# Optimization experiments

Measured on AMD Instinct MI355X. Metric: run time of the kernel, lower is better.

## Reference

```python
import jax, jax.numpy as jnp
import numpy as np

# dims (see shape_source)
N = 100000          # num_ent
E = 400000          # num edges
B = 2048            # batch of (sub, rel) queries
INIT_DIM = 100
UFD = 100           # user_fe_dim
ENT_DIM = INIT_DIM + 3 * UFD   # feature_method='concat' -> 400
H = 2               # attention heads
D = 64              # per-head dim
GCN = H * D         # gcn_dim = embed_dim = 128 (gcn_layer == 1)
NUM_REL = 50
NR2 = 2 * NUM_REL


def setup_inputs() -> dict:
    key = jax.random.key(0)
    ks = jax.random.split(key, 17)
    inp = {}
    # constructor / forward int tensors
    inp["edge_index"] = jax.random.randint(ks[0], (2, E), 0, N, dtype=jnp.int32)
    inp["edge_type"] = jax.random.randint(ks[1], (E,), 0, NR2, dtype=jnp.int32)
    inp["edge_type_p"] = jax.random.randint(ks[2], (E,), 0, NR2, dtype=jnp.int32)
    inp["ent_feature"] = jax.random.randint(ks[3], (N, 3), 0, 3, dtype=jnp.int32)
    inp["sub"] = jax.random.randint(ks[4], (B,), 0, N, dtype=jnp.int32)
    inp["rel"] = jax.random.randint(ks[5], (B,), 0, NR2, dtype=jnp.int32)
    inp["relp"] = jax.random.randint(ks[6], (B,), 0, NR2, dtype=jnp.int32)
    # learned parameters
    s = 0.02
    inp["id_embed"] = jax.random.normal(ks[7], (N, INIT_DIM), jnp.float32) * s
    inp["gender_tab"] = jax.random.normal(ks[8], (3, UFD), jnp.float32) * s
    inp["age_tab"] = jax.random.normal(ks[9], (9, UFD), jnp.float32) * s
    inp["level_tab"] = jax.random.normal(ks[10], (11, UFD), jnp.float32) * s
    inp["init_rel"] = jax.random.normal(ks[11], (NR2, ENT_DIM), jnp.float32) * s
    inp["W"] = jax.random.normal(ks[12], (ENT_DIM, H * D), jnp.float32) * 0.05
    inp["Wr"] = jax.random.normal(ks[13], (ENT_DIM, H * D), jnp.float32) * 0.05
    inp["att_src"] = jax.random.normal(ks[14], (H, D), jnp.float32) * 0.05
    inp["att_dst"] = jax.random.normal(ks[15], (H, D), jnp.float32) * 0.05
    inp["Wrel"] = jax.random.normal(ks[16], (ENT_DIM, GCN), jnp.float32) * 0.05
    return inp


def _segment_softmax(logits, seg, num_segments):
    # logits: [E, H], seg: [E] destination node ids
    m = jax.ops.segment_max(logits, seg, num_segments=num_segments)
    ex = jnp.exp(logits - m[seg])
    den = jax.ops.segment_sum(ex, seg, num_segments=num_segments)
    return ex / (den[seg] + 1e-16)


def _rghat_conv(x, rel_emb, edge_index, edge_type, W, Wr, att_src, att_dst, Wrel):
    # relational multi-head graph attention (RGHATConv)
    n = x.shape[0]
    h = (x @ W).reshape(n, H, D)                       # [N,H,D] projected nodes
    r_proj = (rel_emb @ Wr).reshape(-1, H, D)          # [R,H,D]
    src, dst = edge_index[0], edge_index[1]
    msg = h[src] + r_proj[edge_type]                   # [E,H,D] edge messages
    logits = jax.nn.leaky_relu(
        jnp.sum(msg * att_src, axis=-1) + jnp.sum(h[dst] * att_dst, axis=-1),
        negative_slope=0.2,
    )                                                  # [E,H]
    alpha = _segment_softmax(logits, dst, n)           # per-destination softmax
    out = jax.ops.segment_sum(alpha[..., None] * msg, dst, num_segments=n)
    out = jnp.tanh(out.reshape(n, H * D))              # [N,GCN]
    r_out = rel_emb @ Wrel                             # [R,GCN]
    return out, r_out


def reference(edge_index, edge_type, edge_type_p, ent_feature, sub, rel, relp,
              id_embed, gender_tab, age_tab, level_tab, init_rel,
              W, Wr, att_src, att_dst, Wrel):
    # feature_method == 'concat': gather per-node feature embeddings and concat
    x1 = gender_tab[ent_feature[:, 0]]
    x2 = age_tab[ent_feature[:, 1]]
    x3 = level_tab[ent_feature[:, 2]]
    init_embed = jnp.concatenate([id_embed, x1, x2, x3], axis=1)  # [N, ENT_DIM]
    # single conv layer (gcn_layer == 1); dropouts are identity in eval
    x, r = _rghat_conv(init_embed, init_rel, edge_index, edge_type,
                       W, Wr, att_src, att_dst, Wrel)
    sub_emb = x[sub]                                   # index_select gather
    # add_parent_rel == False -> r returned whole (relp unused)
    return (sub_emb, r, x)
```

## Files before the change

kernel.cpp:

```cpp
#include <hip/hip_runtime.h>
#include <hip/hip_bf16.h>
#include <hip/hip_fp16.h>

#define N_NODES 100000
#define E_EDGES 400000
#define B_SUB 2048
#define INIT_DIM 100
#define UFD 100
#define ENT_DIM 400
#define GCN 128
#define NR2 100
#define KPAD 416
#define NCH 13
#define CAP 64

typedef __attribute__((ext_vector_type(8))) short shortx8;
typedef __attribute__((ext_vector_type(4))) float floatx4;

#define OUT_R_OFF ((long)B_SUB * GCN)
#define OUT_X_OFF ((long)(B_SUB + NR2) * GCN)

__device__ __forceinline__ unsigned short f2b(float f) {
    unsigned u = __float_as_uint(f);
    u += 0x7fffu + ((u >> 16) & 1u);
    return (unsigned short)(u >> 16);
}
__device__ __forceinline__ unsigned pk2(float x, float y) {
    return (unsigned)f2b(x) | ((unsigned)f2b(y) << 16);
}
__device__ __forceinline__ float blo(unsigned u) { return __uint_as_float(u << 16); }
__device__ __forceinline__ float bhi(unsigned u) { return __uint_as_float(u & 0xFFFF0000u); }

__global__ void wt_kernel(const float* __restrict__ W, unsigned short* __restrict__ Wt,
                          int* __restrict__ cursor) {
    int idx = blockIdx.x * 256 + threadIdx.x;
    if (idx < GCN * KPAD) {
        int n = idx & 127, k = idx >> 7;
        unsigned short o = 0;
        if (k < ENT_DIM) o = f2b(W[(long)k * GCN + n]);
        Wt[(long)n * KPAD + k] = o;
    }
    if (idx < N_NODES) cursor[idx] = 0;
}

__global__ void rel_kernel(const float* __restrict__ init_rel, const float* __restrict__ Wr,
                           const float* __restrict__ Wrel, const float* __restrict__ att_src,
                           unsigned* __restrict__ rp_b, float* __restrict__ rproj_att,
                           float* __restrict__ out_r) {
    int rel = blockIdx.x;
    int tx = threadIdx.x;
    __shared__ float rl[ENT_DIM];
    __shared__ float accbuf[128];
    for (int k = tx; k < ENT_DIM; k += 128) rl[k] = init_rel[(long)rel * ENT_DIM + k];
    __syncthreads();
    float acc1 = 0.f, acc2 = 0.f;
    for (int k = 0; k < ENT_DIM; ++k) {
        float v = rl[k];
        acc1 += v * Wr[(long)k * GCN + tx];
        acc2 += v * Wrel[(long)k * GCN + tx];
    }
    out_r[rel * GCN + tx] = acc2;
    accbuf[tx] = acc1;
    int head = tx >> 6, d = tx & 63;
    float v = acc1 * att_src[head * 64 + d];
    for (int off = 32; off > 0; off >>= 1) v += __shfl_down(v, off, 64);
    if (d == 0) rproj_att[rel * 2 + head] = v;
    __syncthreads();
    if (tx < 64) rp_b[rel * 64 + tx] = pk2(accbuf[tx], accbuf[tx + 64]);
}

__device__ __forceinline__ float4 load_seg(const float* __restrict__ id_embed,
                                           const float* __restrict__ gtab,
                                           const float* __restrict__ atab,
                                           const float* __restrict__ ltab,
                                           int n, int f0, int f1, int f2, int kg) {
    if (kg < 100)      return *(const float4*)&id_embed[(long)n * INIT_DIM + kg];
    else if (kg < 200) return *(const float4*)&gtab[f0 * UFD + kg - 100];
    else if (kg < 300) return *(const float4*)&atab[f1 * UFD + kg - 200];
    else if (kg < 400) return *(const float4*)&ltab[f2 * UFD + kg - 300];
    return make_float4(0.f, 0.f, 0.f, 0.f);
}

__global__ __launch_bounds__(256) void hgemm_kernel(
        const float* __restrict__ id_embed, const float* __restrict__ gtab,
        const float* __restrict__ atab, const float* __restrict__ ltab,
        const int* __restrict__ ent_feature, const unsigned short* __restrict__ Wt,
        const float* __restrict__ att_src, const float* __restrict__ att_dst,
        unsigned* __restrict__ h_b, float* __restrict__ hsrc_att, float* __restrict__ hdst_att) {
    __shared__ __align__(16) unsigned short As[64 * 40];
    __shared__ __align__(16) unsigned short Bs[128 * 40];
    __shared__ float attS[128], attD[128];
    int t = threadIdx.x;
    if (t < 128) { attS[t] = att_src[t]; attD[t] = att_dst[t]; }
    int n0 = blockIdx.x * 64;
    int row = t >> 2, seg = t & 3;
    int n = n0 + row;
    bool okn = n < N_NODES;
    int f0 = 0, f1 = 0, f2 = 0;
    if (okn) {
        f0 = ent_feature[n * 3];
        f1 = ent_feature[n * 3 + 1];
        f2 = ent_feature[n * 3 + 2];
    }
    int w = t >> 6, lane = t & 63, quad = lane >> 4, l16 = lane & 15;
    int nB0 = t >> 2,          k00 = (t & 3) * 8;
    int nB1 = (t + 256) >> 2,  k01 = (t & 3) * 8;

    floatx4 acc[8];
#pragma unroll
    for (int c = 0; c < 8; ++c) acc[c] = (floatx4){0.f, 0.f, 0.f, 0.f};

    float4 va = make_float4(0.f, 0.f, 0.f, 0.f), vb = va;
    if (okn) {
        va = load_seg(id_embed, gtab, atab, ltab, n, f0, f1, f2, seg * 8);
        vb = load_seg(id_embed, gtab, atab, ltab, n, f0, f1, f2, seg * 8 + 4);
    }
    shortx8 pb0 = *(const shortx8*)&Wt[(long)nB0 * KPAD + k00];
    shortx8 pb1 = *(const shortx8*)&Wt[(long)nB1 * KPAD + k01];

    for (int ch = 0; ch < NCH; ++ch) {
        uint4 u;
        u.x = pk2(va.x, va.y); u.y = pk2(va.z, va.w);
        u.z = pk2(vb.x, vb.y); u.w = pk2(vb.z, vb.w);
        __syncthreads();
        *(uint4*)&As[row * 40 + seg * 8] = u;
        *(shortx8*)&Bs[nB0 * 40 + k00] = pb0;
        *(shortx8*)&Bs[nB1 * 40 + k01] = pb1;
        if (ch + 1 < NCH) {
            int kg = (ch + 1) * 32 + seg * 8;
            if (okn) {
                va = load_seg(id_embed, gtab, atab, ltab, n, f0, f1, f2, kg);
                vb = load_seg(id_embed, gtab, atab, ltab, n, f0, f1, f2, kg + 4);
            }
            pb0 = *(const shortx8*)&Wt[(long)nB0 * KPAD + (ch + 1) * 32 + k00];
            pb1 = *(const shortx8*)&Wt[(long)nB1 * KPAD + (ch + 1) * 32 + k01];
        }
        __syncthreads();
        shortx8 a = *(shortx8*)&As[(w * 16 + l16) * 40 + quad * 8];
#pragma unroll
        for (int c = 0; c < 8; ++c) {
            shortx8 b = *(shortx8*)&Bs[(c * 16 + l16) * 40 + quad * 8];
            acc[c] = __builtin_amdgcn_mfma_f32_16x16x32_bf16(a, b, acc[c], 0, 0, 0);
        }
    }
    int baseRow = n0 + w * 16 + quad * 4;
#pragma unroll
    for (int i = 0; i < 4; ++i) {
        int node = baseRow + i;
        bool ok = node < N_NODES;
#pragma unroll
        for (int c = 0; c < 4; ++c)
            if (ok) h_b[(long)node * 64 + c * 16 + l16] = pk2(acc[c][i], acc[c + 4][i]);
        float s0 = 0.f, s1 = 0.f, d0 = 0.f, d1 = 0.f;
#pragma unroll
        for (int c = 0; c < 8; ++c) {
            float v = acc[c][i];
            float as_ = attS[c * 16 + l16], ad_ = attD[c * 16 + l16];
            if (c < 4) { s0 += v * as_; d0 += v * ad_; }
            else       { s1 += v * as_; d1 += v * ad_; }
        }
#pragma unroll
        for (int m = 1; m < 16; m <<= 1) {
            s0 += __shfl_xor(s0, m, 64);
            s1 += __shfl_xor(s1, m, 64);
            d0 += __shfl_xor(d0, m, 64);
            d1 += __shfl_xor(d1, m, 64);
        }
        if (ok && l16 == 0) {
            hsrc_att[node * 2] = s0; hsrc_att[node * 2 + 1] = s1;
            hdst_att[node * 2] = d0; hdst_att[node * 2 + 1] = d1;
        }
    }
}

__global__ void fill_kernel(const int* __restrict__ edge_index, const int* __restrict__ edge_type,
                            int* __restrict__ cursor,
                            const float2* __restrict__ hsrc2, const float2* __restrict__ rpa2,
                            const float2* __restrict__ hdst2,
                            uint2* __restrict__ ebuf) {
    int e = blockIdx.x * blockDim.x + threadIdx.x;
    if (e >= E_EDGES) return;
    int src = edge_index[e];
    int dst = edge_index[E_EDGES + e];
    int et = edge_type[e];
    float2 hs = hsrc2[src];
    float2 ra = rpa2[et];
    float2 hd = hdst2[dst];
    float x0 = hs.x + ra.x + hd.x;
    float x1 = hs.y + ra.y + hd.y;
    x0 = x0 > 0.f ? x0 : 0.2f * x0;
    x1 = x1 > 0.f ? x1 : 0.2f * x1;
    __half2 hh = __floats2half2_rn(__expf(x0), __expf(x1));
    union { __half2 h; unsigned u; } cv; cv.h = hh;
    int pos = atomicAdd(&cursor[dst], 1);
    if (pos < CAP)
        ebuf[(long)dst * CAP + pos] = make_uint2(((unsigned)et << 17) | (unsigned)src, cv.u);
}

__global__ __launch_bounds__(256) void agg_kernel(
        const int* __restrict__ cursor, const uint2* __restrict__ ebuf,
        const unsigned* __restrict__ h_b, const unsigned* __restrict__ rp_b,
        float* __restrict__ out_x) {
    int w = threadIdx.x >> 6, l = threadIdx.x & 63;
    int dst = blockIdx.x * 4 + w;
    int cnt = cursor[dst];
    if (cnt > CAP) cnt = CAP;
    const uint2* base = ebuf + (long)dst * CAP;
    float acc0 = 0.f, acc1 = 0.f, den0 = 0.f, den1 = 0.f;
    int j = 0;
    for (; j + 3 < cnt; j += 4) {
        uint2 v0 = base[j], v1 = base[j + 1], v2 = base[j + 2], v3 = base[j + 3];
        union { __half2 h; unsigned u; } c0, c1, c2, c3;
        c0.u = v0.y; c1.u = v1.y; c2.u = v2.y; c3.u = v3.y;
        float2 e0 = __half22float2(c0.h), e1 = __half22float2(c1.h);
        float2 e2 = __half22float2(c2.h), e3 = __half22float2(c3.h);
        unsigned hb0 = h_b[(long)(v0.x & 0x1FFFF) * 64 + l];
        unsigned hb1 = h_b[(long)(v1.x & 0x1FFFF) * 64 + l];
        unsigned hb2 = h_b[(long)(v2.x & 0x1FFFF) * 64 + l];
        unsigned hb3 = h_b[(long)(v3.x & 0x1FFFF) * 64 + l];
        unsigned rb0 = rp_b[(v0.x >> 17) * 64 + l];
        unsigned rb1 = rp_b[(v1.x >> 17) * 64 + l];
        unsigned rb2 = rp_b[(v2.x >> 17) * 64 + l];
        unsigned rb3 = rp_b[(v3.x >> 17) * 64 + l];
        acc0 += e0.x * (blo(hb0) + blo(rb0)) + e1.x * (blo(hb1) + blo(rb1))
              + e2.x * (blo(hb2) + blo(rb2)) + e3.x * (blo(hb3) + blo(rb3));
        acc1 += e0.y * (bhi(hb0) + bhi(rb0)) + e1.y * (bhi(hb1) + bhi(rb1))
              + e2.y * (bhi(hb2) + bhi(rb2)) + e3.y * (bhi(hb3) + bhi(rb3));
        den0 += e0.x + e1.x + e2.x + e3.x;
        den1 += e0.y + e1.y + e2.y + e3.y;
    }
    for (; j < cnt; ++j) {
        uint2 v0 = base[j];
        union { __half2 h; unsigned u; } c0; c0.u = v0.y;
        float2 e0 = __half22float2(c0.h);
        unsigned hb = h_b[(long)(v0.x & 0x1FFFF) * 64 + l];
        unsigned rb = rp_b[(v0.x >> 17) * 64 + l];
        acc0 += e0.x * (blo(hb) + blo(rb));
        acc1 += e0.y * (bhi(hb) + bhi(rb));
        den0 += e0.x;
        den1 += e0.y;
    }
    float i0 = 1.0f / (den0 + 1e-16f), i1 = 1.0f / (den1 + 1e-16f);
    out_x[(long)dst * GCN + l] = tanhf(acc0 * i0);
    out_x[(long)dst * GCN + 64 + l] = tanhf(acc1 * i1);
}

__global__ void gather_kernel(const int* __restrict__ sub, const float* __restrict__ out_x,
                              float* __restrict__ out_sub) {
    int idx = blockIdx.x * blockDim.x + threadIdx.x;
    if (idx >= B_SUB * GCN) return;
    int b = idx >> 7, d = idx & 127;
    out_sub[idx] = out_x[(long)sub[b] * GCN + d];
}

extern "C" void kernel_launch(void* const* d_in, const int* in_sizes, int n_in,
                              void* d_out, int out_size, void* d_ws, size_t ws_size,
                              hipStream_t stream) {
    const int* edge_index = (const int*)d_in[0];
    const int* edge_type  = (const int*)d_in[1];
    const int* ent_feature = (const int*)d_in[3];
    const int* sub = (const int*)d_in[4];
    const float* id_embed = (const float*)d_in[7];
    const float* gtab = (const float*)d_in[8];
    const float* atab = (const float*)d_in[9];
    const float* ltab = (const float*)d_in[10];
    const float* init_rel = (const float*)d_in[11];
    const float* W = (const float*)d_in[12];
    const float* Wr = (const float*)d_in[13];
    const float* att_src = (const float*)d_in[14];
    const float* att_dst = (const float*)d_in[15];
    const float* Wrel = (const float*)d_in[16];

    char* ws = (char*)d_ws;
    unsigned* h_b = (unsigned*)ws;                          ws += (long)N_NODES * 64 * 4;
    unsigned* rp_b = (unsigned*)ws;                         ws += (long)NR2 * 64 * 4;
    float* rproj_att = (float*)ws;                          ws += NR2 * 2 * 4;
    float* hsrc_att = (float*)ws;                           ws += (long)N_NODES * 2 * 4;
    float* hdst_att = (float*)ws;                           ws += (long)N_NODES * 2 * 4;
    unsigned short* Wt = (unsigned short*)ws;               ws += (long)GCN * KPAD * 2;
    int* cursor = (int*)ws;                                 ws += (long)N_NODES * 4;
    uint2* ebuf = (uint2*)ws;                               ws += (long)N_NODES * CAP * 8;

    float* out = (float*)d_out;
    float* out_sub = out;
    float* out_r = out + OUT_R_OFF;
    float* out_x = out + OUT_X_OFF;

    const int NB = (N_NODES + 255) / 256;

    wt_kernel<<<NB, 256, 0, stream>>>(W, Wt, cursor);
    rel_kernel<<<NR2, 128, 0, stream>>>(init_rel, Wr, Wrel, att_src, rp_b, rproj_att, out_r);
    hgemm_kernel<<<(N_NODES + 63) / 64, 256, 0, stream>>>(id_embed, gtab, atab, ltab,
                                                          ent_feature, Wt, att_src, att_dst,
                                                          h_b, hsrc_att, hdst_att);
    fill_kernel<<<(E_EDGES + 255) / 256, 256, 0, stream>>>(edge_index, edge_type, cursor,
                                                           (const float2*)hsrc_att,
                                                           (const float2*)rproj_att,
                                                           (const float2*)hdst_att, ebuf);
    agg_kernel<<<N_NODES / 4, 256, 0, stream>>>(cursor, ebuf, h_b, rp_b, out_x);
    gather_kernel<<<(B_SUB * GCN + 255) / 256, 256, 0, stream>>>(sub, out_x, out_sub);
}
```

Baseline: 242.8 us.

## Restructure node-projection GEMM to stage full weight in LDS via direct loads

The projection GEMM now uses 128-node blocks of 512 threads. Each block copies the whole bf16 weight matrix (128x416) into LDS once with global_load_lds. Each wave loads its A fragments straight into registers, so the per-chunk A staging and the two barriers per K-chunk go away and there is a single barrier before the MFMA loop. The aggregation output stores become nontemporal. In exchange the kernel uses more LDS and registers, which can lower occupancy, and it holds all A values in registers at once.

```diff
diff --git a/kernel.cpp b/kernel.cpp
--- a/kernel.cpp
+++ b/kernel.cpp
@@ -69,80 +69,87 @@
     if (tx < 64) rp_b[rel * 64 + tx] = pk2(accbuf[tx], accbuf[tx + 64]);
 }
 
-__device__ __forceinline__ float4 load_seg(const float* __restrict__ id_embed,
-                                           const float* __restrict__ gtab,
-                                           const float* __restrict__ atab,
-                                           const float* __restrict__ ltab,
-                                           int n, int f0, int f1, int f2, int kg) {
-    if (kg < 100)      return *(const float4*)&id_embed[(long)n * INIT_DIM + kg];
-    else if (kg < 200) return *(const float4*)&gtab[f0 * UFD + kg - 100];
-    else if (kg < 300) return *(const float4*)&atab[f1 * UFD + kg - 200];
-    else if (kg < 400) return *(const float4*)&ltab[f2 * UFD + kg - 300];
-    return make_float4(0.f, 0.f, 0.f, 0.f);
-}
-
-__global__ __launch_bounds__(256) void hgemm_kernel(
+__global__ __launch_bounds__(512) void hgemm_kernel(
         const float* __restrict__ id_embed, const float* __restrict__ gtab,
         const float* __restrict__ atab, const float* __restrict__ ltab,
         const int* __restrict__ ent_feature, const unsigned short* __restrict__ Wt,
         const float* __restrict__ att_src, const float* __restrict__ att_dst,
         unsigned* __restrict__ h_b, float* __restrict__ hsrc_att, float* __restrict__ hdst_att) {
-    __shared__ __align__(16) unsigned short As[64 * 40];
-    __shared__ __align__(16) unsigned short Bs[128 * 40];
-    __shared__ float attS[128], attD[128];
+    __shared__ __align__(16) unsigned short Bs[GCN * KPAD];
+    __shared__ float attS[GCN], attD[GCN];
     int t = threadIdx.x;
-    if (t < 128) { attS[t] = att_src[t]; attD[t] = att_dst[t]; }
-    int n0 = blockIdx.x * 64;
-    int row = t >> 2, seg = t & 3;
-    int n = n0 + row;
-    bool okn = n < N_NODES;
-    int f0 = 0, f1 = 0, f2 = 0;
-    if (okn) {
-        f0 = ent_feature[n * 3];
-        f1 = ent_feature[n * 3 + 1];
-        f2 = ent_feature[n * 3 + 2];
-    }
+    if (t < GCN) { attS[t] = att_src[t]; attD[t] = att_dst[t]; }
     int w = t >> 6, lane = t & 63, quad = lane >> 4, l16 = lane & 15;
-    int nB0 = t >> 2,          k00 = (t & 3) * 8;
-    int nB1 = (t + 256) >> 2,  k01 = (t & 3) * 8;
-
-    floatx4 acc[8];
-#pragma unroll
-    for (int c = 0; c < 8; ++c) acc[c] = (floatx4){0.f, 0.f, 0.f, 0.f};
-
-    float4 va = make_float4(0.f, 0.f, 0.f, 0.f), vb = va;
-    if (okn) {
-        va = load_seg(id_embed, gtab, atab, ltab, n, f0, f1, f2, seg * 8);
-        vb = load_seg(id_embed, gtab, atab, ltab, n, f0, f1, f2, seg * 8 + 4);
-    }
-    shortx8 pb0 = *(const shortx8*)&Wt[(long)nB0 * KPAD + k00];
-    shortx8 pb1 = *(const shortx8*)&Wt[(long)nB1 * KPAD + k01];
-
+    int n0 = blockIdx.x * 128;
+    int nrow = n0 + w * 16 + l16;
+    int nclamp = nrow < N_NODES ? nrow : N_NODES - 1;
+    int f0 = ent_feature[nclamp * 3];
+    int f1 = ent_feature[nclamp * 3 + 1];
+    int f2 = ent_feature[nclamp * 3 + 2];
+    const float* pid = id_embed + (long)nclamp * INIT_DIM;
+    const float* pg = gtab + f0 * UFD;
+    const float* pa = atab + f1 * UFD;
+    const float* pl = ltab + f2 * UFD;
+
+    float4 va[NCH], vb[NCH];
+#pragma unroll
+    for (int ch = 0; ch < NCH; ++ch) {
+        int kg = ch * 32 + quad * 8;
+        const float* p0;
+        if (kg < 100)      p0 = pid + kg;
+        else if (kg < 200) p0 = pg + kg - 100;
+        else if (kg < 300) p0 = pa + kg - 200;
+        else if (kg < 400) p0 = pl + kg - 300;
+        else               p0 = pid;
+        va[ch] = *(const float4*)p0;
+        int k4 = kg + 4;
+        const float* p1;
+        if (k4 < 100)      p1 = pid + k4;
+        else if (k4 < 200) p1 = pg + k4 - 100;
+        else if (k4 < 300) p1 = pa + k4 - 200;
+        else if (k4 < 400) p1 = pl + k4 - 300;
+        else               p1 = pid;
+        vb[ch] = *(const float4*)p1;
+    }
+
+    {
+        const char* gsrc = (const char*)Wt;
+        char* lbase = (char*)Bs;
+#pragma unroll
+        for (int i = 0; i < NCH; ++i) {
+            int off = i * 8192 + w * 1024;
+            __builtin_amdgcn_global_load_lds(
+                (const __attribute__((address_space(1))) unsigned int*)(gsrc + off + lane * 16),
+                (__attribute__((address_space(3))) unsigned int*)(lbase + off), 16, 0, 0);
+        }
+    }
+
+    shortx8 aF[NCH];
+#pragma unroll
     for (int ch = 0; ch < NCH; ++ch) {
         uint4 u;
-        u.x = pk2(va.x, va.y); u.y = pk2(va.z, va.w);
-        u.z = pk2(vb.x, vb.y); u.w = pk2(vb.z, vb.w);
-        __syncthreads();
-        *(uint4*)&As[row * 40 + seg * 8] = u;
-        *(shortx8*)&Bs[nB0 * 40 + k00] = pb0;
-        *(shortx8*)&Bs[nB1 * 40 + k01] = pb1;
-        if (ch + 1 < NCH) {
-            int kg = (ch + 1) * 32 + seg * 8;
-            if (okn) {
-                va = load_seg(id_embed, gtab, atab, ltab, n, f0, f1, f2, kg);
-                vb = load_seg(id_embed, gtab, atab, ltab, n, f0, f1, f2, kg + 4);
-            }
-            pb0 = *(const shortx8*)&Wt[(long)nB0 * KPAD + (ch + 1) * 32 + k00];
-            pb1 = *(const shortx8*)&Wt[(long)nB1 * KPAD + (ch + 1) * 32 + k01];
-        }
-        __syncthreads();
-        shortx8 a = *(shortx8*)&As[(w * 16 + l16) * 40 + quad * 8];
+        u.x = pk2(va[ch].x, va[ch].y);
+        u.y = pk2(va[ch].z, va[ch].w);
+        u.z = pk2(vb[ch].x, vb[ch].y);
+        u.w = pk2(vb[ch].z, vb[ch].w);
+        aF[ch] = *(shortx8*)&u;
+    }
+    floatx4 acc[8];
+#pragma unroll
+    for (int c = 0; c < 8; ++c) acc[c] = (floatx4){0.f, 0.f, 0.f, 0.f};
+
+    __syncthreads();
+
+    const unsigned short* bp = &Bs[l16 * KPAD + quad * 8];
+#pragma unroll
+    for (int ch = 0; ch < NCH; ++ch) {
 #pragma unroll
         for (int c = 0; c < 8; ++c) {
-            shortx8 b = *(shortx8*)&Bs[(c * 16 + l16) * 40 + quad * 8];
-            acc[c] = __builtin_amdgcn_mfma_f32_16x16x32_bf16(a, b, acc[c], 0, 0, 0);
-        }
-    }
+            shortx8 b = *(const shortx8*)&bp[c * 16 * KPAD + ch * 32];
+            acc[c] = __builtin_amdgcn_mfma_f32_16x16x32_bf16(aF[ch], b, acc[c], 0, 0, 0);
+        }
+    }
+
     int baseRow = n0 + w * 16 + quad * 4;
 #pragma unroll
     for (int i = 0; i < 4; ++i) {
@@ -241,8 +248,8 @@
         den1 += e0.y;
     }
     float i0 = 1.0f / (den0 + 1e-16f), i1 = 1.0f / (den1 + 1e-16f);
-    out_x[(long)dst * GCN + l] = tanhf(acc0 * i0);
-    out_x[(long)dst * GCN + 64 + l] = tanhf(acc1 * i1);
+    __builtin_nontemporal_store(tanhf(acc0 * i0), &out_x[(long)dst * GCN + l]);
+    __builtin_nontemporal_store(tanhf(acc1 * i1), &out_x[(long)dst * GCN + 64 + l]);
 }
 
 __global__ void gather_kernel(const int* __restrict__ sub, const float* __restrict__ out_x,
@@ -290,9 +297,9 @@
 
     wt_kernel<<<NB, 256, 0, stream>>>(W, Wt, cursor);
     rel_kernel<<<NR2, 128, 0, stream>>>(init_rel, Wr, Wrel, att_src, rp_b, rproj_att, out_r);
-    hgemm_kernel<<<(N_NODES + 63) / 64, 256, 0, stream>>>(id_embed, gtab, atab, ltab,
-                                                          ent_feature, Wt, att_src, att_dst,
-                                                          h_b, hsrc_att, hdst_att);
+    hgemm_kernel<<<(N_NODES + 127) / 128, 512, 0, stream>>>(id_embed, gtab, atab, ltab,
+                                                            ent_feature, Wt, att_src, att_dst,
+                                                            h_b, hsrc_att, hdst_att);
     fill_kernel<<<(E_EDGES + 255) / 256, 256, 0, stream>>>(edge_index, edge_type, cursor,
                                                            (const float2*)hsrc_att,
                                                            (const float2*)rproj_att,
```

Measured after the change: 246.9 us. Within noise of the previous version (+1.7%).
